# Optimization experiments

Hardware: AMD Instinct MI355X
Metric: run time of the kernel (lower is better)

Reference implementation:

```python
import jax, jax.numpy as jnp
import numpy as np

N, H, W, C = 2, 96, 96, 256
HEADS, P = 8, 25
DH = C // HEADS
HID = int(C * 4.0)


def _ln(x, g, b):
    m = jnp.mean(x, axis=-1, keepdims=True)
    v = jnp.var(x, axis=-1, keepdims=True)
    return (x - m) / jnp.sqrt(v + 1e-5) * g + b


def _deform_sample(value, loc, h, w):
    # value: (n, heads, h*w, dh); loc: (n, Lq, heads, P, 2) normalized to [0,1] (x,y)
    # Bilinear sampling with align_corners=False and zero padding, as in
    # grid_sample used by MSDeformAttn.
    n = value.shape[0]
    gx = loc[..., 0] * w - 0.5
    gy = loc[..., 1] * h - 0.5
    x0 = jnp.floor(gx)
    y0 = jnp.floor(gy)
    fx = gx - x0
    fy = gy - y0
    out = jnp.zeros((n, HEADS, gx.shape[1] * P, DH), dtype=value.dtype)
    for dx, dy in ((0, 0), (1, 0), (0, 1), (1, 1)):
        xi = x0 + dx
        yi = y0 + dy
        wgt = (fx if dx else 1.0 - fx) * (fy if dy else 1.0 - fy)
        valid = ((xi >= 0) & (xi <= w - 1) & (yi >= 0) & (yi <= h - 1)).astype(value.dtype)
        xi_c = jnp.clip(xi, 0, w - 1).astype(jnp.int32)
        yi_c = jnp.clip(yi, 0, h - 1).astype(jnp.int32)
        idx = yi_c * w + xi_c                                   # (n, Lq, heads, P)
        idx = jnp.transpose(idx, (0, 2, 1, 3)).reshape(n, HEADS, -1)
        g = jnp.take_along_axis(value, idx[..., None], axis=2)  # (n, heads, Lq*P, dh)
        wv = jnp.transpose(wgt * valid, (0, 2, 1, 3)).reshape(n, HEADS, -1, 1)
        out = out + g * wv
    return out


def setup_inputs() -> dict:
    key = jax.random.key(0)
    ks = jax.random.split(key, 20)
    s = 0.02
    inp = {
        'x': jax.random.normal(ks[0], (N, H, W, C), jnp.float32),
        'ref_points': jax.random.uniform(ks[1], (N, H * W, 1, 2), jnp.float32),
        'spatial_shapes': jnp.array([[H, W]], dtype=jnp.int32),
        'level_start_index': jnp.zeros((1,), dtype=jnp.int32),
        'ln1_g': jnp.ones((C,), jnp.float32),
        'ln1_b': jnp.zeros((C,), jnp.float32),
        'w_off': jax.random.normal(ks[2], (C, HEADS * P * 2), jnp.float32) * s,
        'b_off': jax.random.normal(ks[3], (HEADS * P * 2,), jnp.float32) * s,
        'w_attn': jax.random.normal(ks[4], (C, HEADS * P), jnp.float32) * s,
        'b_attn': jax.random.normal(ks[5], (HEADS * P,), jnp.float32) * s,
        'w_val': jax.random.normal(ks[6], (C, C), jnp.float32) * s,
        'b_val': jnp.zeros((C,), jnp.float32),
        'w_out': jax.random.normal(ks[7], (C, C), jnp.float32) * s,
        'b_out': jnp.zeros((C,), jnp.float32),
        'ln2_g': jnp.ones((C,), jnp.float32),
        'ln2_b': jnp.zeros((C,), jnp.float32),
        'w_fc1': jax.random.normal(ks[8], (C, HID), jnp.float32) * s,
        'b_fc1': jnp.zeros((HID,), jnp.float32),
        'w_fc2': jax.random.normal(ks[9], (HID, C), jnp.float32) * s,
        'b_fc2': jnp.zeros((C,), jnp.float32),
    }
    return inp


def reference(x, ref_points, spatial_shapes, level_start_index,
              ln1_g, ln1_b, w_off, b_off, w_attn, b_attn,
              w_val, b_val, w_out, b_out, ln2_g, ln2_b,
              w_fc1, b_fc1, w_fc2, b_fc2):
    n, h, w, c = x.shape
    lq = h * w
    shortcut = x
    # pre-norm + flatten to query
    q = _ln(x, ln1_g, ln1_b).reshape(n, lq, c)
    # MSDeformAttn (n_levels = 1)
    value = (q @ w_val + b_val).reshape(n, lq, HEADS, DH).transpose(0, 2, 1, 3)
    off = (q @ w_off + b_off).reshape(n, lq, HEADS, P, 2)
    aw = jax.nn.softmax((q @ w_attn + b_attn).reshape(n, lq, HEADS, P), axis=-1)
    norm = jnp.array([w, h], dtype=x.dtype)          # offsets normalized by (W, H)
    ref = ref_points[:, :, 0, :]                     # (n, Lq, 2)
    loc = ref[:, :, None, None, :] + off / norm      # (n, Lq, heads, P, 2)
    sampled = _deform_sample(value, loc, h, w).reshape(n, HEADS, lq, P, DH)
    attn = jnp.einsum('nqhp,nhqpd->nqhd', aw, sampled).reshape(n, lq, c)
    attn = attn @ w_out + b_out
    x1 = shortcut + attn.reshape(n, h, w, c)
    # MLP block
    y = _ln(x1, ln2_g, ln2_b)
    y = jax.nn.gelu(y @ w_fc1 + b_fc1, approximate=False) @ w_fc2 + b_fc2
    return x1 + y
```

## Files before the change

kernel.cpp:

```cpp
#include <hip/hip_runtime.h>
#include <hip/hip_bf16.h>
#include <math.h>

typedef __hip_bfloat16 bf16;
typedef __attribute__((ext_vector_type(8))) short short8;
typedef __attribute__((ext_vector_type(4))) float f32x4;

#define NB 2
#define HH 96
#define WW 96
#define CC 256
#define NHEADS 8
#define PP 25
#define DHH 32
#define HIDN 1024
#define LQ (HH*WW)
#define TT (NB*LQ)
#define NCAT 640

__device__ __forceinline__ float b2f(bf16 v){ return __bfloat162float(v); }
__device__ __forceinline__ bf16  f2b(float v){ return __float2bfloat16(v); }
__device__ __forceinline__ float lo_bf(unsigned u){ return __uint_as_float(u << 16); }
__device__ __forceinline__ float hi_bf(unsigned u){ return __uint_as_float(u & 0xffff0000u); }

__device__ __forceinline__ void gl2lds16(const void* g, void* l) {
    __builtin_amdgcn_global_load_lds(
        (const __attribute__((address_space(1))) unsigned int*)g,
        (__attribute__((address_space(3))) unsigned int*)l, 16, 0, 0);
}

__global__ __launch_bounds__(256) void prep_t(const float* __restrict__ src,
                                              bf16* __restrict__ dst,
                                              int Klog2, int total)
{
    int idx = blockIdx.x*256 + threadIdx.x;
    if (idx >= total) return;
    int K = 1 << Klog2;
    int n = idx >> Klog2, k = idx & (K-1);
    int N = total >> Klog2;
    dst[idx] = f2b(src[(size_t)k*N + n]);
}

__global__ __launch_bounds__(256) void prep_cat(const float* __restrict__ w_off,
                                                const float* __restrict__ w_attn,
                                                const float* __restrict__ b_off,
                                                const float* __restrict__ b_attn,
                                                bf16* __restrict__ wcatT,
                                                float* __restrict__ bcat)
{
    int idx = blockIdx.x*256 + threadIdx.x;
    if (idx >= NCAT*CC) return;
    int n = idx >> 8, k = idx & 255;
    float v = (n < 400) ? w_off[(size_t)k*400 + n]
            : (n < 600) ? w_attn[(size_t)k*200 + (n-400)] : 0.f;
    wcatT[idx] = f2b(v);
    if (idx < NCAT)
        bcat[idx] = (idx < 400) ? b_off[idx] : (idx < 600 ? b_attn[idx-400] : 0.f);
}

__global__ __launch_bounds__(256) void ln_kernel(const float* __restrict__ x,
                                                 const float* __restrict__ g,
                                                 const float* __restrict__ b,
                                                 bf16* __restrict__ out)
{
    const int t = blockIdx.x*4 + (threadIdx.x >> 6);
    const int l = threadIdx.x & 63;
    const float4 v = *(const float4*)(x + (size_t)t*CC + l*4);
    float s  = v.x + v.y + v.z + v.w;
    float s2 = v.x*v.x + v.y*v.y + v.z*v.z + v.w*v.w;
    #pragma unroll
    for (int m = 1; m < 64; m <<= 1) { s += __shfl_xor(s, m); s2 += __shfl_xor(s2, m); }
    const float mean = s * (1.f/CC);
    const float var  = s2 * (1.f/CC) - mean*mean;
    const float rs   = 1.f / sqrtf(var + 1e-5f);
    const float4 gg = *(const float4*)(g + l*4);
    const float4 bb = *(const float4*)(b + l*4);
    bf16 o[4];
    o[0] = f2b((v.x-mean)*rs*gg.x + bb.x);
    o[1] = f2b((v.y-mean)*rs*gg.y + bb.y);
    o[2] = f2b((v.z-mean)*rs*gg.z + bb.z);
    o[3] = f2b((v.w-mean)*rs*gg.w + bb.w);
    *(uint2*)(out + (size_t)t*CC + l*4) = *(uint2*)o;
}

template<int EPI>
__global__ __launch_bounds__(256) void mfma_gemm(const bf16* __restrict__ A,
                                                 const bf16* __restrict__ Bt,
                                                 const float* __restrict__ bias,
                                                 void* __restrict__ outv,
                                                 const float* __restrict__ resid,
                                                 int K, int N)
{
    __shared__ short As[128*64];
    __shared__ short Bs[128*64];
    const int tid = threadIdx.x;
    const int w = tid >> 6, l = tid & 63;
    const int bm = blockIdx.x, bn = blockIdx.y;

    const bf16* sbase[8];
    short*      lbase[8];
    {
        const int lrow = l >> 3;
        const int q    = (l & 7) ^ lrow;
        #pragma unroll
        for (int j = 0; j < 8; j++) {
            int r = w*8 + j;
            bool isA = r < 16;
            int rr = isA ? r : r - 16;
            int row = rr*8 + lrow;
            size_t grow = (size_t)((isA ? bm : bn)*128 + row);
            sbase[j] = (isA ? A : Bt) + grow*K + q*8;
            lbase[j] = (isA ? As : Bs) + rr*512;
        }
    }

    int aoff[2][4], boff[2][4];
    #pragma unroll
    for (int s = 0; s < 2; s++)
        #pragma unroll
        for (int i = 0; i < 4; i++) {
            int q = s*4 + (l >> 4);
            int m = 64*(w >> 1) + i*16 + (l & 15);
            int n = 64*(w &  1) + i*16 + (l & 15);
            aoff[s][i] = (m*8 + (q ^ (m & 7))) * 8;
            boff[s][i] = (n*8 + (q ^ (n & 7))) * 8;
        }

    f32x4 acc[4][4];
    #pragma unroll
    for (int i = 0; i < 4; i++)
        #pragma unroll
        for (int j = 0; j < 4; j++)
            acc[i][j] = (f32x4){0.f, 0.f, 0.f, 0.f};

    for (int k0 = 0; k0 < K; k0 += 64) {
        #pragma unroll
        for (int j = 0; j < 8; j++)
            gl2lds16(sbase[j] + k0, lbase[j]);
        __syncthreads();
        #pragma unroll
        for (int s = 0; s < 2; s++) {
            short8 af[4], bfr[4];
            #pragma unroll
            for (int i = 0; i < 4; i++) {
                af[i]  = *(const short8*)(As + aoff[s][i]);
                bfr[i] = *(const short8*)(Bs + boff[s][i]);
            }
            #pragma unroll
            for (int i = 0; i < 4; i++)
                #pragma unroll
                for (int j = 0; j < 4; j++)
                    acc[i][j] = __builtin_amdgcn_mfma_f32_16x16x32_bf16(af[i], bfr[j], acc[i][j], 0, 0, 0);
        }
        __syncthreads();
    }

    const int row0 = bm*128 + 64*(w >> 1) + (l >> 4)*4;
    const int col0 = bn*128 + 64*(w &  1) + (l & 15);
    #pragma unroll
    for (int i = 0; i < 4; i++) {
        #pragma unroll
        for (int j = 0; j < 4; j++) {
            const int col = col0 + j*16;
            const float bs = bias[col];
            #pragma unroll
            for (int r = 0; r < 4; r++) {
                const int row = row0 + i*16 + r;
                float v = acc[i][j][r] + bs;
                size_t o = (size_t)row * N + col;
                if (EPI == 0) {
                    ((bf16*)outv)[o] = f2b(v);
                } else if (EPI == 2) {
                    ((bf16*)outv)[o] = f2b(0.5f * v * (1.f + erff(v * 0.70710678118654752f)));
                } else {
                    ((float*)outv)[o] = v + resid[o];
                }
            }
        }
    }
}

__global__ __launch_bounds__(256) void softmax_kernel(bf16* __restrict__ cat)
{
    const int gid = blockIdx.x*256 + threadIdx.x;
    if (gid >= TT*NHEADS) return;
    bf16* p = cat + (size_t)(gid >> 3)*NCAT + 400 + (gid & 7)*PP;
    float e[PP];
    float m = b2f(p[0]);
    #pragma unroll
    for (int i = 1; i < PP; i++) m = fmaxf(m, b2f(p[i]));
    float s = 0.f;
    #pragma unroll
    for (int i = 0; i < PP; i++) { e[i] = expf(b2f(p[i]) - m); s += e[i]; }
    const float inv = 1.f / s;
    #pragma unroll
    for (int i = 0; i < PP; i++) p[i] = f2b(e[i] * inv);
}

__global__ __launch_bounds__(256) void sample_kernel(const bf16* __restrict__ val,
                                                     const bf16* __restrict__ cat,
                                                     const float* __restrict__ refp,
                                                     bf16* __restrict__ samp)
{
    const int t     = blockIdx.x*4 + (threadIdx.x >> 6);
    const int l     = threadIdx.x & 63;
    const int hh    = l >> 3;
    const int lane8 = l & 7;
    const int c0    = hh*DHH + lane8*4;
    const int n     = (t >= LQ) ? 1 : 0;

    const float rx96 = refp[(size_t)t*2 + 0] * 96.f - 0.5f;
    const float ry96 = refp[(size_t)t*2 + 1] * 96.f - 0.5f;
    const bf16* row  = cat + (size_t)t*NCAT;
    const unsigned* offp = (const unsigned*)(row + hh*(PP*2));
    const bf16* awp  = row + 400 + hh*PP;
    const bf16* vbase = val + (size_t)n*LQ*CC + c0;

    float a0 = 0.f, a1 = 0.f, a2 = 0.f, a3 = 0.f;
    for (int p = 0; p < PP; p++) {
        const float a = b2f(awp[p]);
        const unsigned uo = offp[p];
        const float gx = rx96 + lo_bf(uo);
        const float gy = ry96 + hi_bf(uo);
        const float x0f = floorf(gx), y0f = floorf(gy);
        const float fx = gx - x0f, fy = gy - y0f;
        const int ix = (int)x0f, iy = (int)y0f;
        const float ax1 = a * fx, ax0 = a - ax1;
        #pragma unroll
        for (int d = 0; d < 4; d++) {
            const int dx = d & 1, dy = d >> 1;
            const int xi = ix + dx, yi = iy + dy;
            const float wt = (dx ? ax1 : ax0) * (dy ? fy : 1.f - fy);
            const bool valid = (xi >= 0) & (xi <= WW-1) & (yi >= 0) & (yi <= HH-1);
            const int xc = min(max(xi, 0), WW-1);
            const int yc = min(max(yi, 0), HH-1);
            const float wv = valid ? wt : 0.f;
            const uint2 vv = *(const uint2*)(vbase + (size_t)(yc*WW + xc)*CC);
            a0 += wv * lo_bf(vv.x);
            a1 += wv * hi_bf(vv.x);
            a2 += wv * lo_bf(vv.y);
            a3 += wv * hi_bf(vv.y);
        }
    }
    bf16 o[4] = { f2b(a0), f2b(a1), f2b(a2), f2b(a3) };
    *(uint2*)(samp + (size_t)t*CC + c0) = *(uint2*)o;
}

extern "C" void kernel_launch(void* const* d_in, const int* in_sizes, int n_in,
                              void* d_out, int out_size, void* d_ws, size_t ws_size,
                              hipStream_t stream)
{
    const float* x      = (const float*)d_in[0];
    const float* refp   = (const float*)d_in[1];
    const float* ln1_g  = (const float*)d_in[4];
    const float* ln1_b  = (const float*)d_in[5];
    const float* w_off  = (const float*)d_in[6];
    const float* b_off  = (const float*)d_in[7];
    const float* w_attn = (const float*)d_in[8];
    const float* b_attn = (const float*)d_in[9];
    const float* w_val  = (const float*)d_in[10];
    const float* b_val  = (const float*)d_in[11];
    const float* w_out  = (const float*)d_in[12];
    const float* b_out  = (const float*)d_in[13];
    const float* ln2_g  = (const float*)d_in[14];
    const float* ln2_b  = (const float*)d_in[15];
    const float* w_fc1  = (const float*)d_in[16];
    const float* b_fc1  = (const float*)d_in[17];
    const float* w_fc2  = (const float*)d_in[18];
    const float* b_fc2  = (const float*)d_in[19];

    char* wsb = (char*)d_ws;
    bf16*  q     = (bf16*)(wsb + 0);
    bf16*  val   = (bf16*)(wsb + 9437184);
    bf16*  cat   = (bf16*)(wsb + 18874368);
    bf16*  samp  = (bf16*)(wsb + 42467328);
    float* x1    = (float*)(wsb + 51904512);
    bf16*  wvalT = (bf16*)(wsb + 70778880);
    bf16*  woutT = (bf16*)(wsb + 70909952);
    bf16*  wfc1T = (bf16*)(wsb + 71041024);
    bf16*  wfc2T = (bf16*)(wsb + 71565312);
    bf16*  wcatT = (bf16*)(wsb + 72089600);
    float* bcat  = (float*)(wsb + 72417280);
    bf16*  hid   = (bf16*)(wsb + 0);
    bf16*  y0    = samp;

    if (ws_size < 72419840) return;

    const dim3 blk(256);
    prep_t<<<dim3((65536 +255)/256), blk, 0, stream>>>(w_val, wvalT, 8, 65536);
    prep_t<<<dim3((65536 +255)/256), blk, 0, stream>>>(w_out, woutT, 8, 65536);
    prep_t<<<dim3((262144+255)/256), blk, 0, stream>>>(w_fc1, wfc1T, 8, 262144);
    prep_t<<<dim3((262144+255)/256), blk, 0, stream>>>(w_fc2, wfc2T, 10, 262144);
    prep_cat<<<dim3((NCAT*CC+255)/256), blk, 0, stream>>>(w_off, w_attn, b_off, b_attn, wcatT, bcat);

    ln_kernel<<<dim3(TT/4), blk, 0, stream>>>(x, ln1_g, ln1_b, q);
    mfma_gemm<0><<<dim3(TT/128, CC/128),   blk, 0, stream>>>(q, wvalT, b_val, (void*)val, nullptr, CC, CC);
    mfma_gemm<0><<<dim3(TT/128, NCAT/128), blk, 0, stream>>>(q, wcatT, bcat,  (void*)cat, nullptr, CC, NCAT);
    softmax_kernel<<<dim3(TT*NHEADS/256), blk, 0, stream>>>(cat);
    sample_kernel<<<dim3(TT/4), blk, 0, stream>>>(val, cat, refp, samp);
    mfma_gemm<3><<<dim3(TT/128, CC/128),   blk, 0, stream>>>(samp, woutT, b_out, (void*)x1, x, CC, CC);
    ln_kernel<<<dim3(TT/4), blk, 0, stream>>>(x1, ln2_g, ln2_b, y0);
    mfma_gemm<2><<<dim3(TT/128, HIDN/128), blk, 0, stream>>>(y0, wfc1T, b_fc1, (void*)hid, nullptr, CC, HIDN);
    mfma_gemm<3><<<dim3(TT/128, CC/128),   blk, 0, stream>>>(hid, wfc2T, b_fc2, d_out, x1, HIDN, CC);
}
```

Before: 296.4 us.

## Fuse value and offset/attn GEMMs, merge weight prep, restructure deformable sampling

Concatenates the value projection with the offset/attention projection into one GEMM producing a 896-wide row, and collapses the five weight-transpose launches into one prep kernel. The sampling kernel now precomputes bilinear weights and indices per block into LDS. It then gathers 8 channels per lane with 16-byte loads, and a swizzled block order groups queries for locality. This cuts launch count and GEMM passes over q and widens gathers. The value rows are now strided by 896 rather than 256, which may hurt gather cache efficiency.

```diff
diff --git a/kernel.cpp b/kernel.cpp
--- a/kernel.cpp
+++ b/kernel.cpp
@@ -16,7 +16,8 @@
 #define HIDN 1024
 #define LQ (HH*WW)
 #define TT (NB*LQ)
-#define NCAT 640
+#define NVC 896
+#define TB 8
 
 __device__ __forceinline__ float b2f(bf16 v){ return __bfloat162float(v); }
 __device__ __forceinline__ bf16  f2b(float v){ return __float2bfloat16(v); }
@@ -29,33 +30,42 @@
         (__attribute__((address_space(3))) unsigned int*)l, 16, 0, 0);
 }
 
-__global__ __launch_bounds__(256) void prep_t(const float* __restrict__ src,
-                                              bf16* __restrict__ dst,
-                                              int Klog2, int total)
-{
-    int idx = blockIdx.x*256 + threadIdx.x;
-    if (idx >= total) return;
-    int K = 1 << Klog2;
-    int n = idx >> Klog2, k = idx & (K-1);
-    int N = total >> Klog2;
-    dst[idx] = f2b(src[(size_t)k*N + n]);
-}
-
-__global__ __launch_bounds__(256) void prep_cat(const float* __restrict__ w_off,
+__global__ __launch_bounds__(256) void prep_all(const float* __restrict__ w_val,
+                                                const float* __restrict__ w_off,
                                                 const float* __restrict__ w_attn,
+                                                const float* __restrict__ w_fc1,
+                                                const float* __restrict__ w_fc2,
+                                                const float* __restrict__ w_out,
+                                                const float* __restrict__ b_val,
                                                 const float* __restrict__ b_off,
                                                 const float* __restrict__ b_attn,
-                                                bf16* __restrict__ wcatT,
-                                                float* __restrict__ bcat)
-{
-    int idx = blockIdx.x*256 + threadIdx.x;
-    if (idx >= NCAT*CC) return;
-    int n = idx >> 8, k = idx & 255;
-    float v = (n < 400) ? w_off[(size_t)k*400 + n]
-            : (n < 600) ? w_attn[(size_t)k*200 + (n-400)] : 0.f;
-    wcatT[idx] = f2b(v);
-    if (idx < NCAT)
-        bcat[idx] = (idx < 400) ? b_off[idx] : (idx < 600 ? b_attn[idx-400] : 0.f);
+                                                bf16* __restrict__ wvcT,
+                                                bf16* __restrict__ wfc1T,
+                                                bf16* __restrict__ wfc2T,
+                                                bf16* __restrict__ woutT,
+                                                float* __restrict__ bvc)
+{
+    const int idx = blockIdx.x*256 + threadIdx.x;
+    if (idx < 229376) {
+        int n = idx >> 8, k = idx & 255;
+        float v = (n < 256) ? w_val[(size_t)k*256 + n]
+                : (n < 656) ? w_off[(size_t)k*400 + (n-256)]
+                : (n < 856) ? w_attn[(size_t)k*200 + (n-656)] : 0.f;
+        wvcT[idx] = f2b(v);
+    } else if (idx < 491520) {
+        int j = idx - 229376; int n = j >> 8, k = j & 255;
+        wfc1T[j] = f2b(w_fc1[(size_t)k*1024 + n]);
+    } else if (idx < 753664) {
+        int j = idx - 491520; int n = j >> 10, k = j & 1023;
+        wfc2T[j] = f2b(w_fc2[(size_t)k*256 + n]);
+    } else if (idx < 819200) {
+        int j = idx - 753664; int n = j >> 8, k = j & 255;
+        woutT[j] = f2b(w_out[(size_t)k*256 + n]);
+    }
+    if (idx < NVC)
+        bvc[idx] = (idx < 256) ? b_val[idx]
+                 : (idx < 656) ? b_off[idx-256]
+                 : (idx < 856) ? b_attn[idx-656] : 0.f;
 }
 
 __global__ __launch_bounds__(256) void ln_kernel(const float* __restrict__ x,
@@ -180,11 +190,11 @@
     }
 }
 
-__global__ __launch_bounds__(256) void softmax_kernel(bf16* __restrict__ cat)
+__global__ __launch_bounds__(256) void softmax_kernel(bf16* __restrict__ vc)
 {
     const int gid = blockIdx.x*256 + threadIdx.x;
     if (gid >= TT*NHEADS) return;
-    bf16* p = cat + (size_t)(gid >> 3)*NCAT + 400 + (gid & 7)*PP;
+    bf16* p = vc + (size_t)(gid >> 3)*NVC + 656 + (gid & 7)*PP;
     float e[PP];
     float m = b2f(p[0]);
     #pragma unroll
@@ -197,53 +207,77 @@
     for (int i = 0; i < PP; i++) p[i] = f2b(e[i] * inv);
 }
 
-__global__ __launch_bounds__(256) void sample_kernel(const bf16* __restrict__ val,
-                                                     const bf16* __restrict__ cat,
+__global__ __launch_bounds__(256) void sample_kernel(const bf16* __restrict__ vc,
                                                      const float* __restrict__ refp,
                                                      bf16* __restrict__ samp)
 {
-    const int t     = blockIdx.x*4 + (threadIdx.x >> 6);
-    const int l     = threadIdx.x & 63;
-    const int hh    = l >> 3;
-    const int lane8 = l & 7;
-    const int c0    = hh*DHH + lane8*4;
-    const int n     = (t >= LQ) ? 1 : 0;
-
-    const float rx96 = refp[(size_t)t*2 + 0] * 96.f - 0.5f;
-    const float ry96 = refp[(size_t)t*2 + 1] * 96.f - 0.5f;
-    const bf16* row  = cat + (size_t)t*NCAT;
-    const unsigned* offp = (const unsigned*)(row + hh*(PP*2));
-    const bf16* awp  = row + 400 + hh*PP;
-    const bf16* vbase = val + (size_t)n*LQ*CC + c0;
-
-    float a0 = 0.f, a1 = 0.f, a2 = 0.f, a3 = 0.f;
-    for (int p = 0; p < PP; p++) {
-        const float a = b2f(awp[p]);
-        const unsigned uo = offp[p];
-        const float gx = rx96 + lo_bf(uo);
-        const float gy = ry96 + hi_bf(uo);
+    __shared__ float4  w4[TB*200];
+    __shared__ ushort4 i4[TB*200];
+    const int b = blockIdx.x;
+    const int tbase = ((b & 7)*288 + (b >> 3)) * TB;
+    const int tid = threadIdx.x;
+
+    for (int i = tid; i < TB*200; i += 256) {
+        const int tl  = (i*5243) >> 20;
+        const int rem = i - tl*200;
+        const int h   = (rem*41) >> 10;
+        const int p   = rem - h*25;
+        const int t   = tbase + tl;
+        const bf16* row = vc + (size_t)t*NVC;
+        const unsigned uo = *(const unsigned*)(row + 256 + h*50 + 2*p);
+        const float a  = b2f(row[656 + h*25 + p]);
+        const float gx = refp[(size_t)t*2+0]*96.f - 0.5f + lo_bf(uo);
+        const float gy = refp[(size_t)t*2+1]*96.f - 0.5f + hi_bf(uo);
         const float x0f = floorf(gx), y0f = floorf(gy);
         const float fx = gx - x0f, fy = gy - y0f;
         const int ix = (int)x0f, iy = (int)y0f;
-        const float ax1 = a * fx, ax0 = a - ax1;
+        float  wv[4];
+        ushort ii[4];
         #pragma unroll
         for (int d = 0; d < 4; d++) {
             const int dx = d & 1, dy = d >> 1;
             const int xi = ix + dx, yi = iy + dy;
-            const float wt = (dx ? ax1 : ax0) * (dy ? fy : 1.f - fy);
             const bool valid = (xi >= 0) & (xi <= WW-1) & (yi >= 0) & (yi <= HH-1);
             const int xc = min(max(xi, 0), WW-1);
             const int yc = min(max(yi, 0), HH-1);
-            const float wv = valid ? wt : 0.f;
-            const uint2 vv = *(const uint2*)(vbase + (size_t)(yc*WW + xc)*CC);
-            a0 += wv * lo_bf(vv.x);
-            a1 += wv * hi_bf(vv.x);
-            a2 += wv * lo_bf(vv.y);
-            a3 += wv * hi_bf(vv.y);
-        }
-    }
-    bf16 o[4] = { f2b(a0), f2b(a1), f2b(a2), f2b(a3) };
-    *(uint2*)(samp + (size_t)t*CC + c0) = *(uint2*)o;
+            ii[d] = (ushort)(yc*WW + xc);
+            wv[d] = valid ? a * (dx ? fx : 1.f-fx) * (dy ? fy : 1.f-fy) : 0.f;
+        }
+        w4[i] = (float4){wv[0], wv[1], wv[2], wv[3]};
+        i4[i] = (ushort4){ii[0], ii[1], ii[2], ii[3]};
+    }
+    __syncthreads();
+
+    const int wv_ = tid >> 6, l = tid & 63;
+    const int tl  = wv_*2 + (l >> 5);
+    const int r   = l & 31;
+    const int h   = r >> 2, oct = r & 3;
+    const int c0  = h*DHH + oct*8;
+    const int t   = tbase + tl;
+    const int n   = (t >= LQ) ? 1 : 0;
+    const bf16* pv = vc + (size_t)n*LQ*NVC + c0;
+    const int pib = tl*200 + h*25;
+
+    float acc[8] = {0.f,0.f,0.f,0.f,0.f,0.f,0.f,0.f};
+    for (int p = 0; p < PP; p++) {
+        const float4  w  = w4[pib + p];
+        const ushort4 id = i4[pib + p];
+        const float  wt_[4] = {w.x, w.y, w.z, w.w};
+        const ushort id_[4] = {id.x, id.y, id.z, id.w};
+        #pragma unroll
+        for (int d = 0; d < 4; d++) {
+            const float wt = wt_[d];
+            const uint4 vv = *(const uint4*)(pv + (size_t)id_[d]*NVC);
+            acc[0] += wt*lo_bf(vv.x); acc[1] += wt*hi_bf(vv.x);
+            acc[2] += wt*lo_bf(vv.y); acc[3] += wt*hi_bf(vv.y);
+            acc[4] += wt*lo_bf(vv.z); acc[5] += wt*hi_bf(vv.z);
+            acc[6] += wt*lo_bf(vv.w); acc[7] += wt*hi_bf(vv.w);
+        }
+    }
+    bf16 o[8];
+    #pragma unroll
+    for (int j = 0; j < 8; j++) o[j] = f2b(acc[j]);
+    *(uint4*)(samp + (size_t)t*CC + c0) = *(uint4*)o;
 }
 
 extern "C" void kernel_launch(void* const* d_in, const int* in_sizes, int n_in,
@@ -271,33 +305,27 @@
 
     char* wsb = (char*)d_ws;
     bf16*  q     = (bf16*)(wsb + 0);
-    bf16*  val   = (bf16*)(wsb + 9437184);
-    bf16*  cat   = (bf16*)(wsb + 18874368);
+    bf16*  vc    = (bf16*)(wsb + 9437184);
     bf16*  samp  = (bf16*)(wsb + 42467328);
     float* x1    = (float*)(wsb + 51904512);
-    bf16*  wvalT = (bf16*)(wsb + 70778880);
-    bf16*  woutT = (bf16*)(wsb + 70909952);
-    bf16*  wfc1T = (bf16*)(wsb + 71041024);
-    bf16*  wfc2T = (bf16*)(wsb + 71565312);
-    bf16*  wcatT = (bf16*)(wsb + 72089600);
-    float* bcat  = (float*)(wsb + 72417280);
+    bf16*  wvcT  = (bf16*)(wsb + 70778880);
+    bf16*  wfc1T = (bf16*)(wsb + 71237632);
+    bf16*  wfc2T = (bf16*)(wsb + 71761920);
+    bf16*  woutT = (bf16*)(wsb + 72286208);
+    float* bvc   = (float*)(wsb + 72417280);
     bf16*  hid   = (bf16*)(wsb + 0);
     bf16*  y0    = samp;
 
-    if (ws_size < 72419840) return;
+    if (ws_size < 72420864) return;
 
     const dim3 blk(256);
-    prep_t<<<dim3((65536 +255)/256), blk, 0, stream>>>(w_val, wvalT, 8, 65536);
-    prep_t<<<dim3((65536 +255)/256), blk, 0, stream>>>(w_out, woutT, 8, 65536);
-    prep_t<<<dim3((262144+255)/256), blk, 0, stream>>>(w_fc1, wfc1T, 8, 262144);
-    prep_t<<<dim3((262144+255)/256), blk, 0, stream>>>(w_fc2, wfc2T, 10, 262144);
-    prep_cat<<<dim3((NCAT*CC+255)/256), blk, 0, stream>>>(w_off, w_attn, b_off, b_attn, wcatT, bcat);
-
+    prep_all<<<dim3(3200), blk, 0, stream>>>(w_val, w_off, w_attn, w_fc1, w_fc2, w_out,
+                                             b_val, b_off, b_attn,
+                                             wvcT, wfc1T, wfc2T, woutT, bvc);
     ln_kernel<<<dim3(TT/4), blk, 0, stream>>>(x, ln1_g, ln1_b, q);
-    mfma_gemm<0><<<dim3(TT/128, CC/128),   blk, 0, stream>>>(q, wvalT, b_val, (void*)val, nullptr, CC, CC);
-    mfma_gemm<0><<<dim3(TT/128, NCAT/128), blk, 0, stream>>>(q, wcatT, bcat,  (void*)cat, nullptr, CC, NCAT);
-    softmax_kernel<<<dim3(TT*NHEADS/256), blk, 0, stream>>>(cat);
-    sample_kernel<<<dim3(TT/4), blk, 0, stream>>>(val, cat, refp, samp);
+    mfma_gemm<0><<<dim3(TT/128, NVC/128), blk, 0, stream>>>(q, wvcT, bvc, (void*)vc, nullptr, CC, NVC);
+    softmax_kernel<<<dim3(TT*NHEADS/256), blk, 0, stream>>>(vc);
+    sample_kernel<<<dim3(TT/TB), blk, 0, stream>>>(vc, refp, samp);
     mfma_gemm<3><<<dim3(TT/128, CC/128),   blk, 0, stream>>>(samp, woutT, b_out, (void*)x1, x, CC, CC);
     ln_kernel<<<dim3(TT/4), blk, 0, stream>>>(x1, ln2_g, ln2_b, y0);
     mfma_gemm<2><<<dim3(TT/128, HIDN/128), blk, 0, stream>>>(y0, wfc1T, b_fc1, (void*)hid, nullptr, CC, HIDN);
```

Result: faster. 265.5 us (-10.4%).
